# Kernel optimization log

Measured on AMD Instinct MI355X. Metric: run time of the kernel, lower is better.

## Reference

```python
import jax, jax.numpy as jnp
import numpy as np

N_NODES = 100000
N_EDGES = 1200000
N_GRAPHS = 256
IN_DIM = 15
HID = 64


def setup_inputs() -> dict:
    key = jax.random.key(0)
    ks = jax.random.split(key, 12)
    x = jax.random.normal(ks[0], (N_NODES, IN_DIM), dtype=jnp.float32)
    edge_index = jax.random.randint(ks[1], (2, N_EDGES), 0, N_NODES, dtype=jnp.int64)
    batch = jnp.sort(jax.random.randint(ks[2], (N_NODES,), 0, N_GRAPHS, dtype=jnp.int64))
    def glorot(k, fan_in, fan_out):
        lim = jnp.sqrt(6.0 / (fan_in + fan_out)).astype(jnp.float32)
        return jax.random.uniform(k, (fan_in, fan_out), jnp.float32, -lim, lim)
    return {
        'x': x, 'edge_index': edge_index, 'batch': batch,
        'W1': glorot(ks[3], IN_DIM, HID), 'b1': jnp.zeros((HID,), jnp.float32),
        'W2': glorot(ks[4], HID, HID),    'b2': jnp.zeros((HID,), jnp.float32),
        'W3': glorot(ks[5], HID, HID),    'b3': jnp.zeros((HID,), jnp.float32),
        'W4': glorot(ks[6], HID, HID),    'b4': jnp.zeros((HID,), jnp.float32),
    }


def _gcn_conv(x, src, dst, norm, W, b):
    # GCNConv: h = x @ W; out[dst] += norm * h[src]; out += b
    h = x @ W                      # [N, out]
    msg = h[src] * norm[:, None]   # [E+N, out] gather + scale
    out = jax.ops.segment_sum(msg, dst, num_segments=N_NODES)
    return out + b


def reference(x, edge_index, batch, W1, b1, W2, b2, W3, b3, W4, b4):
    # gcn_norm with self-loops (PyG default): A_hat = D^-1/2 (A+I) D^-1/2
    loop = jnp.arange(N_NODES, dtype=edge_index.dtype)
    src = jnp.concatenate([edge_index[0], loop])
    dst = jnp.concatenate([edge_index[1], loop])
    deg = jax.ops.segment_sum(jnp.ones_like(src, dtype=x.dtype), dst, num_segments=N_NODES)
    dinv = jnp.where(deg > 0, jax.lax.rsqrt(deg), 0.0)
    norm = dinv[src] * dinv[dst]   # [E+N]

    h = jax.nn.relu(_gcn_conv(x, src, dst, norm, W1, b1))
    h = jax.nn.relu(_gcn_conv(h, src, dst, norm, W2, b2))
    h = jax.nn.relu(_gcn_conv(h, src, dst, norm, W3, b3))
    h = jax.nn.relu(_gcn_conv(h, src, dst, norm, W4, b4))

    # global_mean_pool over batch ids
    sums = jax.ops.segment_sum(h, batch, num_segments=N_GRAPHS)
    cnt = jax.ops.segment_sum(jnp.ones((N_NODES,), h.dtype), batch, num_segments=N_GRAPHS)
    return sums / jnp.maximum(cnt, 1.0)[:, None]
```

## Files before the change

### kernel.cpp

```cpp
#include <hip/hip_runtime.h>
#include <hip/hip_bf16.h>

#define NN 100000
#define NE 1200000
#define NG 256
#define NB 256
#define BSZ 391
#define NBK1 128
#define ECH 9376
#define MAXB 6144
#define NBND_BLK 391
#define NPAD_BLK 6250

typedef __attribute__((ext_vector_type(8))) short bf16x8;
typedef __attribute__((ext_vector_type(4))) float f32x4;

__device__ __forceinline__ unsigned f2b(float f) {
    unsigned b = __float_as_uint(f);
    return (b + 0x7FFFu + ((b >> 16) & 1u)) >> 16;
}
__device__ __forceinline__ float b2f(unsigned short u) {
    return __uint_as_float((unsigned)u << 16);
}
__device__ __forceinline__ float4 b2f4(ushort4 u) {
    return make_float4(b2f(u.x), b2f(u.y), b2f(u.z), b2f(u.w));
}
__device__ __forceinline__ void add_u4(float* a, uint4 v) {
    const unsigned* u = (const unsigned*)&v;
#pragma unroll
    for (int i = 0; i < 4; ++i) {
        a[2*i]   += __uint_as_float(u[i] << 16);
        a[2*i+1] += __uint_as_float(u[i] & 0xFFFF0000u);
    }
}

__global__ void ph0_hist(const int* __restrict__ dst, int* __restrict__ hrows) {
    __shared__ int h[NB];
    const int t = threadIdx.x;
    h[t] = 0;
    __syncthreads();
    const int e0 = blockIdx.x * ECH;
    const int cnt = min(ECH, NE - e0);
    for (int i = t; i < cnt; i += 256)
        atomicAdd(&h[dst[e0 + i] / BSZ], 1);
    __syncthreads();
    hrows[blockIdx.x * NB + t] = h[t];
}

__global__ void ph_scan(const int* __restrict__ hrows, int* __restrict__ chunkoff,
                        int* __restrict__ bbase, int* __restrict__ row_off) {
    __shared__ int s[NB];
    const int t = threadIdx.x;
    int run = 0;
    for (int b = 0; b < NBK1; ++b) {
        int v = hrows[b * NB + t];
        chunkoff[b * NB + t] = run;
        run += v;
    }
    s[t] = run;
    __syncthreads();
    for (int off = 1; off < NB; off <<= 1) {
        int u = (t >= off) ? s[t - off] : 0;
        __syncthreads();
        s[t] += u;
        __syncthreads();
    }
    const int excl = s[t] - run;
    bbase[t] = excl;
    for (int b = 0; b < NBK1; ++b) chunkoff[b * NB + t] += excl;
    if (t == NB - 1) { bbase[NB] = NE; row_off[NN] = NE; }
}

__global__ void ph1_bucketize(const int* __restrict__ src, const int* __restrict__ dst,
                              const int* __restrict__ chunkoff, unsigned* __restrict__ barray) {
    __shared__ int lbase[NB];
    __shared__ int lcur[NB];
    const int t = threadIdx.x;
    lbase[t] = chunkoff[blockIdx.x * NB + t];
    lcur[t] = 0;
    __syncthreads();
    const int e0 = blockIdx.x * ECH;
    const int cnt = min(ECH, NE - e0);
    for (int i = t; i < cnt; i += 256) {
        int d = dst[e0 + i], s = src[e0 + i];
        int b = d / BSZ;
        int pos = lbase[b] + atomicAdd(&lcur[b], 1);
        barray[pos] = ((unsigned)(d - b * BSZ) << 17) | (unsigned)s;
    }
}

__global__ void ph2_build(const unsigned* __restrict__ barray, const int* __restrict__ bbase,
                          int* __restrict__ row_off, float* __restrict__ dinv,
                          int* __restrict__ csr) {
    __shared__ unsigned estage[MAXB];
    __shared__ int lcsr[MAXB];
    __shared__ int s[512];
    __shared__ int cur[BSZ];
    const int t = threadIdx.x;
    const int b = blockIdx.x;
    const int ebase = bbase[b];
    const int cnt = bbase[b + 1] - ebase;
    const int nbase = b * BSZ;
    const int nnodes = min(BSZ, NN - nbase);
    s[t] = 0; s[t + 256] = 0;
    __syncthreads();
    for (int i = t; i < cnt; i += 256) {
        unsigned e = barray[ebase + i];
        estage[i] = e;
        atomicAdd(&s[e >> 17], 1);
    }
    __syncthreads();
    for (int off = 1; off < 512; off <<= 1) {
        int v1 = (t >= off) ? s[t - off] : 0;
        int v2 = s[t + 256 - off];
        __syncthreads();
        s[t] += v1; s[t + 256] += v2;
        __syncthreads();
    }
    for (int l = t; l < nnodes; l += 256) {
        int incl = s[l];
        int excl = l ? s[l - 1] : 0;
        row_off[nbase + l] = ebase + excl;
        dinv[nbase + l] = rsqrtf((float)(incl - excl) + 1.0f);
        cur[l] = excl;
    }
    __syncthreads();
    for (int i = t; i < cnt; i += 256) {
        unsigned e = estage[i];
        int pos = atomicAdd(&cur[e >> 17], 1);
        lcsr[pos] = (int)(e & 0x1FFFFu);
    }
    __syncthreads();
    for (int i = t; i < cnt; i += 256)
        csr[ebase + i] = lcsr[i];
}

__global__ void k_prep(const float* __restrict__ W2, const float* __restrict__ W3,
                       const float* __restrict__ W4, unsigned short* __restrict__ wt,
                       const float* __restrict__ x, const float* __restrict__ dinv,
                       unsigned short* __restrict__ xs,
                       const int* __restrict__ batch, int* __restrict__ gstart) {
    const int blk = blockIdx.x;
    const int t = threadIdx.x;
    if (blk < 3) {
        const float* W = (blk == 0) ? W2 : (blk == 1) ? W3 : W4;
        unsigned short* o = wt + blk * 8192;
        const int n = t >> 2;
        const int j0 = (t & 3) * 16;
#pragma unroll
        for (int j = 0; j < 16; ++j) {
            float wv = W[(j0 + j) * 64 + n];
            unsigned short h = (unsigned short)f2b(wv);
            o[n * 64 + j0 + j] = h;
            o[4096 + n * 64 + j0 + j] = (unsigned short)f2b(wv - b2f(h));
        }
    } else if (blk < 3 + NBND_BLK) {
        int i = (blk - 3) * 256 + t;
        if (i >= NN) return;
        int b = batch[i];
        if (i == 0) {
            for (int g = 0; g <= b; ++g) gstart[g] = 0;
        } else {
            int bp = batch[i - 1];
            for (int g = bp + 1; g <= b; ++g) gstart[g] = i;
        }
        if (i == NN - 1) {
            for (int g = b + 1; g <= NG; ++g) gstart[g] = NN;
        }
    } else {
        int i = (blk - 3 - NBND_BLK) * 256 + t;
        if (i < NN * 16) {
            int n = i >> 4, k = i & 15;
            float v = (k < 15) ? dinv[n] * x[n * 15 + k] : 0.f;
            xs[i] = (unsigned short)f2b(v);
        }
    }
}

__global__ void fused1(const unsigned short* __restrict__ xs, const int* __restrict__ row_off,
                       const int* __restrict__ csr, const float* __restrict__ dinv,
                       const float* __restrict__ W, const float* __restrict__ bias,
                       unsigned* __restrict__ out) {
    __shared__ float4 Wl[16][16];
    __shared__ float  al[64][20];
    const int t = threadIdx.x;
    if (t < 240) Wl[t >> 4][t & 15] = ((const float4*)W)[t];
    if (t < 16) Wl[15][t] = make_float4(0,0,0,0);
    const int nl = t >> 2, c4 = t & 3;
    const int node = blockIdx.x * 64 + nl;
    float4 acc = make_float4(0,0,0,0);
    float dv = 0.f;
    if (node < NN) {
        const ushort4* base = (const ushort4*)xs;
        acc = b2f4(base[(size_t)node * 4 + c4]);
        int p = row_off[node], e = row_off[node + 1];
        for (; p + 3 < e; p += 4) {
            int s0 = csr[p], s1 = csr[p+1], s2 = csr[p+2], s3 = csr[p+3];
            float4 a = b2f4(base[(size_t)s0 * 4 + c4]);
            float4 b = b2f4(base[(size_t)s1 * 4 + c4]);
            float4 c = b2f4(base[(size_t)s2 * 4 + c4]);
            float4 d = b2f4(base[(size_t)s3 * 4 + c4]);
            acc.x += (a.x + b.x) + (c.x + d.x);
            acc.y += (a.y + b.y) + (c.y + d.y);
            acc.z += (a.z + b.z) + (c.z + d.z);
            acc.w += (a.w + b.w) + (c.w + d.w);
        }
        for (; p < e; ++p) {
            float4 a = b2f4(base[(size_t)csr[p] * 4 + c4]);
            acc.x += a.x; acc.y += a.y; acc.z += a.z; acc.w += a.w;
        }
        dv = dinv[node];
        acc.x *= dv; acc.y *= dv; acc.z *= dv; acc.w *= dv;
    }
    ((float4*)&al[nl][0])[c4] = acc;
    __syncthreads();
    if (node >= NN) return;
    float4 o0 = ((const float4*)bias)[c4 * 4 + 0];
    float4 o1 = ((const float4*)bias)[c4 * 4 + 1];
    float4 o2 = ((const float4*)bias)[c4 * 4 + 2];
    float4 o3 = ((const float4*)bias)[c4 * 4 + 3];
#pragma unroll
    for (int k = 0; k < 16; ++k) {
        float a = al[nl][k];
        float4 w0 = Wl[k][c4 * 4 + 0];
        float4 w1 = Wl[k][c4 * 4 + 1];
        float4 w2 = Wl[k][c4 * 4 + 2];
        float4 w3 = Wl[k][c4 * 4 + 3];
        o0.x = fmaf(a, w0.x, o0.x); o0.y = fmaf(a, w0.y, o0.y); o0.z = fmaf(a, w0.z, o0.z); o0.w = fmaf(a, w0.w, o0.w);
        o1.x = fmaf(a, w1.x, o1.x); o1.y = fmaf(a, w1.y, o1.y); o1.z = fmaf(a, w1.z, o1.z); o1.w = fmaf(a, w1.w, o1.w);
        o2.x = fmaf(a, w2.x, o2.x); o2.y = fmaf(a, w2.y, o2.y); o2.z = fmaf(a, w2.z, o2.z); o2.w = fmaf(a, w2.w, o2.w);
        o3.x = fmaf(a, w3.x, o3.x); o3.y = fmaf(a, w3.y, o3.y); o3.z = fmaf(a, w3.z, o3.z); o3.w = fmaf(a, w3.w, o3.w);
    }
    float dv2 = dv;
    o0.x = fmaxf(o0.x, 0.f) * dv2; o0.y = fmaxf(o0.y, 0.f) * dv2; o0.z = fmaxf(o0.z, 0.f) * dv2; o0.w = fmaxf(o0.w, 0.f) * dv2;
    o1.x = fmaxf(o1.x, 0.f) * dv2; o1.y = fmaxf(o1.y, 0.f) * dv2; o1.z = fmaxf(o1.z, 0.f) * dv2; o1.w = fmaxf(o1.w, 0.f) * dv2;
    o2.x = fmaxf(o2.x, 0.f) * dv2; o2.y = fmaxf(o2.y, 0.f) * dv2; o2.z = fmaxf(o2.z, 0.f) * dv2; o2.w = fmaxf(o2.w, 0.f) * dv2;
    o3.x = fmaxf(o3.x, 0.f) * dv2; o3.y = fmaxf(o3.y, 0.f) * dv2; o3.z = fmaxf(o3.z, 0.f) * dv2; o3.w = fmaxf(o3.w, 0.f) * dv2;
    uint4 lo, hi;
    lo.x = f2b(o0.x) | (f2b(o0.y) << 16);
    lo.y = f2b(o0.z) | (f2b(o0.w) << 16);
    lo.z = f2b(o1.x) | (f2b(o1.y) << 16);
    lo.w = f2b(o1.z) | (f2b(o1.w) << 16);
    hi.x = f2b(o2.x) | (f2b(o2.y) << 16);
    hi.y = f2b(o2.z) | (f2b(o2.w) << 16);
    hi.z = f2b(o3.x) | (f2b(o3.y) << 16);
    hi.w = f2b(o3.z) | (f2b(o3.w) << 16);
    uint4* ob = (uint4*)out + (size_t)node * 8 + c4 * 2;
    ob[0] = lo; ob[1] = hi;
}

template <bool LAST>
__global__ __launch_bounds__(256) void fused64(const unsigned short* __restrict__ g,
                        const int* __restrict__ row_off, const int* __restrict__ csr,
                        const float* __restrict__ dinv, const unsigned short* __restrict__ wt,
                        const float* __restrict__ bias, void* __restrict__ outv) {
    __shared__ alignas(16) unsigned short Ahi[16][72];
    __shared__ alignas(16) unsigned short Alo[16][72];
    __shared__ alignas(16) float dinv_l[16];
    const int t = threadIdx.x;

    const int nl = t >> 4;
    const int s8 = (t >> 3) & 1;
    const int q  = t & 7;
    const int node = blockIdx.x * 16 + nl;
    float acc[8] = {0,0,0,0,0,0,0,0};
    const float dv = dinv[node];
    {
        const uint4* fbase = (const uint4*)g;
        const int r0 = row_off[node], r1 = row_off[node + 1];
        const int half = (r1 - r0 + 1) >> 1;
        int p = r0 + s8 * half;
        const int e = s8 ? r1 : (r0 + half);
        if (s8 == 0) add_u4(acc, fbase[(size_t)node * 8 + q]);
        int i0 = csr[p],   i1 = csr[p+1], i2 = csr[p+2], i3 = csr[p+3];
        int i4 = csr[p+4], i5 = csr[p+5], i6 = csr[p+6], i7 = csr[p+7];
        while (p < e) {
            const int rem = e - p;
            uint4 v0, v1, v2, v3, v4, v5, v6, v7;
            v0 = fbase[(size_t)i0 * 8 + q];
            if (rem > 1) v1 = fbase[(size_t)i1 * 8 + q];
            if (rem > 2) v2 = fbase[(size_t)i2 * 8 + q];
            if (rem > 3) v3 = fbase[(size_t)i3 * 8 + q];
            if (rem > 4) v4 = fbase[(size_t)i4 * 8 + q];
            if (rem > 5) v5 = fbase[(size_t)i5 * 8 + q];
            if (rem > 6) v6 = fbase[(size_t)i6 * 8 + q];
            if (rem > 7) v7 = fbase[(size_t)i7 * 8 + q];
            p += 8;
            i0 = csr[p];   i1 = csr[p+1]; i2 = csr[p+2]; i3 = csr[p+3];
            i4 = csr[p+4]; i5 = csr[p+5]; i6 = csr[p+6]; i7 = csr[p+7];
            add_u4(acc, v0);
            if (rem > 1) add_u4(acc, v1);
            if (rem > 2) add_u4(acc, v2);
            if (rem > 3) add_u4(acc, v3);
            if (rem > 4) add_u4(acc, v4);
            if (rem > 5) add_u4(acc, v5);
            if (rem > 6) add_u4(acc, v6);
            if (rem > 7) add_u4(acc, v7);
        }
    }
#pragma unroll
    for (int i = 0; i < 8; ++i) acc[i] += __shfl_xor(acc[i], 8, 64);
    if (s8 == 0) {
        uint4 uh, ul;
        unsigned* uhp = (unsigned*)&uh;
        unsigned* ulp = (unsigned*)&ul;
#pragma unroll
        for (int i = 0; i < 4; ++i) {
            float va = acc[2*i] * dv;
            float vb = acc[2*i+1] * dv;
            unsigned ha = f2b(va), hb = f2b(vb);
            unsigned la = f2b(va - b2f((unsigned short)ha));
            unsigned lb = f2b(vb - b2f((unsigned short)hb));
            uhp[i] = ha | (hb << 16);
            ulp[i] = la | (lb << 16);
        }
        *(uint4*)&Ahi[nl][q * 8] = uh;
        *(uint4*)&Alo[nl][q * 8] = ul;
        if (q == 0) dinv_l[nl] = dv;
    }
    const int wid = t >> 6;
    const int l = t & 63;
    const int rr = l & 15;
    const int kb = l >> 4;
    const unsigned short* wrow = wt + (wid * 16 + rr) * 64;
    bf16x8 bh0 = *(const bf16x8*)(wrow + kb * 8);
    bf16x8 bh1 = *(const bf16x8*)(wrow + 32 + kb * 8);
    bf16x8 bl0 = *(const bf16x8*)(wrow + 4096 + kb * 8);
    bf16x8 bl1 = *(const bf16x8*)(wrow + 4096 + 32 + kb * 8);
    __syncthreads();

    f32x4 c = {0.f, 0.f, 0.f, 0.f};
    {
        bf16x8 ah0 = *(const bf16x8*)&Ahi[rr][kb * 8];
        bf16x8 am0 = *(const bf16x8*)&Alo[rr][kb * 8];
        c = __builtin_amdgcn_mfma_f32_16x16x32_bf16(ah0, bh0, c, 0, 0, 0);
        c = __builtin_amdgcn_mfma_f32_16x16x32_bf16(ah0, bl0, c, 0, 0, 0);
        c = __builtin_amdgcn_mfma_f32_16x16x32_bf16(am0, bh0, c, 0, 0, 0);
        bf16x8 ah1 = *(const bf16x8*)&Ahi[rr][32 + kb * 8];
        bf16x8 am1 = *(const bf16x8*)&Alo[rr][32 + kb * 8];
        c = __builtin_amdgcn_mfma_f32_16x16x32_bf16(ah1, bh1, c, 0, 0, 0);
        c = __builtin_amdgcn_mfma_f32_16x16x32_bf16(ah1, bl1, c, 0, 0, 0);
        c = __builtin_amdgcn_mfma_f32_16x16x32_bf16(am1, bh1, c, 0, 0, 0);
    }
    float bv = bias[wid * 16 + rr];
    float4 dq = *(const float4*)&dinv_l[kb * 4];
    const float* dqp = (const float*)&dq;
#pragma unroll
    for (int r = 0; r < 4; ++r) {
        int nd = blockIdx.x * 16 + kb * 4 + r;
        float o = fmaxf(c[r] + bv, 0.f);
        if (!LAST) {
            o *= dqp[r];
            ((unsigned short*)outv)[(size_t)nd * 64 + wid * 16 + rr] = (unsigned short)f2b(o);
        } else {
            ((float*)outv)[(size_t)nd * 64 + wid * 16 + rr] = o;
        }
    }
}

__global__ void k_pool(const float* __restrict__ h, const int* __restrict__ gstart,
                       float* __restrict__ out) {
    __shared__ float s[4][64];
    int g = blockIdx.x;
    int t = threadIdx.x, lane = t & 63, w = t >> 6;
    int r0 = gstart[g], r1 = gstart[g + 1];
    float acc = 0.f;
    for (int r = r0 + w; r < r1; r += 4) acc += h[(size_t)r * 64 + lane];
    s[w][lane] = acc;
    __syncthreads();
    if (t < 64) {
        float v = s[0][t] + s[1][t] + s[2][t] + s[3][t];
        float c = (float)(r1 - r0);
        out[g * 64 + t] = v / fmaxf(c, 1.f);
    }
}

static inline size_t al256(size_t x) { return (x + 255) & ~(size_t)255; }

extern "C" void kernel_launch(void* const* d_in, const int* in_sizes, int n_in,
                              void* d_out, int out_size, void* d_ws, size_t ws_size,
                              hipStream_t stream) {
    const float* x     = (const float*)d_in[0];
    const int*   eidx  = (const int*)d_in[1];
    const int*   batch = (const int*)d_in[2];
    const float* W1 = (const float*)d_in[3];  const float* b1 = (const float*)d_in[4];
    const float* W2 = (const float*)d_in[5];  const float* b2 = (const float*)d_in[6];
    const float* W3 = (const float*)d_in[7];  const float* b3 = (const float*)d_in[8];
    const float* W4 = (const float*)d_in[9];  const float* b4 = (const float*)d_in[10];
    float* out = (float*)d_out;
    (void)in_sizes; (void)n_in; (void)out_size; (void)ws_size;

    const int* src = eidx;
    const int* dst = eidx + NE;

    char* p = (char*)d_ws;
    size_t off = 0;
    int*   hrows   = (int*)(p + off);   off = al256(off + sizeof(int) * NBK1 * NB);
    int*   chunkoff= (int*)(p + off);   off = al256(off + sizeof(int) * NBK1 * NB);
    int*   bbase   = (int*)(p + off);   off = al256(off + sizeof(int) * (NB + 1));
    int*   gstart  = (int*)(p + off);   off = al256(off + sizeof(int) * (NG + 1));
    int*   row_off = (int*)(p + off);   off = al256(off + sizeof(int) * (NN + 1));
    float* dinv    = (float*)(p + off); off = al256(off + sizeof(float) * NN);
    unsigned short* wt = (unsigned short*)(p + off); off = al256(off + sizeof(short) * 3 * 8192);
    int*   csr     = (int*)(p + off);   off = al256(off + sizeof(int) * (NE + 16));
    unsigned short* F0 = (unsigned short*)(p + off); off = al256(off + sizeof(short) * (size_t)NN * 64);
    unsigned short* F1 = (unsigned short*)(p + off); off = al256(off + sizeof(short) * (size_t)NN * 64);
    float* H4      = (float*)(p + off); off = al256(off + sizeof(float) * (size_t)NN * 64);
    unsigned*       barray = (unsigned*)H4;
    unsigned short* xs     = F1;

    ph0_hist     <<<NBK1, 256, 0, stream>>>(dst, hrows);
    ph_scan      <<<1, NB, 0, stream>>>(hrows, chunkoff, bbase, row_off);
    ph1_bucketize<<<NBK1, 256, 0, stream>>>(src, dst, chunkoff, barray);
    ph2_build    <<<NB, 256, 0, stream>>>(barray, bbase, row_off, dinv, csr);
    k_prep       <<<3 + NBND_BLK + NPAD_BLK, 256, 0, stream>>>(W2, W3, W4, wt, x, dinv, xs, batch, gstart);

    fused1        <<<(NN + 63) / 64, 256, 0, stream>>>(xs, row_off, csr, dinv, W1, b1, (unsigned*)F0);
    fused64<false><<<NN / 16, 256, 0, stream>>>(F0, row_off, csr, dinv, wt,        b2, F1);
    fused64<false><<<NN / 16, 256, 0, stream>>>(F1, row_off, csr, dinv, wt + 8192, b3, F0);
    fused64<true> <<<NN / 16, 256, 0, stream>>>(F0, row_off, csr, dinv, wt + 16384,b4, H4);

    k_pool  <<<NG, 256, 0, stream>>>(H4, gstart, out);
}
```

Before: 208.2 us.

## Parallelize bucket offset scan and stage weights in LDS for fused64

The single-block serial scan over 128 chunk histograms is split into a 256-block parallel column scan plus a small second-level scan. Bucketize now adds the bucket base to each chunk offset itself. Separately, fused64 cooperatively copies the full hi/lo bf16 weight matrix into padded shared memory and has each wave read its MFMA B operands from LDS rather than from per-lane global loads. This adds one kernel launch and about 18KB of LDS per block, which may reduce occupancy of the gather-heavy fused kernels.

```diff
diff --git a/kernel.cpp b/kernel.cpp
--- a/kernel.cpp
+++ b/kernel.cpp
@@ -47,17 +47,30 @@
     hrows[blockIdx.x * NB + t] = h[t];
 }
 
-__global__ void ph_scan(const int* __restrict__ hrows, int* __restrict__ chunkoff,
-                        int* __restrict__ bbase, int* __restrict__ row_off) {
+__global__ void ph_scanA(const int* __restrict__ hrows, int* __restrict__ chunkoff,
+                         int* __restrict__ btot) {
+    __shared__ int s[NBK1];
+    const int b = threadIdx.x;
+    const int t = blockIdx.x;
+    int v = hrows[b * NB + t];
+    s[b] = v;
+    __syncthreads();
+    for (int off = 1; off < NBK1; off <<= 1) {
+        int u = (b >= off) ? s[b - off] : 0;
+        __syncthreads();
+        s[b] += u;
+        __syncthreads();
+    }
+    chunkoff[b * NB + t] = s[b] - v;
+    if (b == NBK1 - 1) btot[t] = s[b];
+}
+
+__global__ void ph_scanB(const int* __restrict__ btot, int* __restrict__ bbase,
+                         int* __restrict__ row_off) {
     __shared__ int s[NB];
     const int t = threadIdx.x;
-    int run = 0;
-    for (int b = 0; b < NBK1; ++b) {
-        int v = hrows[b * NB + t];
-        chunkoff[b * NB + t] = run;
-        run += v;
-    }
-    s[t] = run;
+    int v = btot[t];
+    s[t] = v;
     __syncthreads();
     for (int off = 1; off < NB; off <<= 1) {
         int u = (t >= off) ? s[t - off] : 0;
@@ -65,18 +78,17 @@
         s[t] += u;
         __syncthreads();
     }
-    const int excl = s[t] - run;
-    bbase[t] = excl;
-    for (int b = 0; b < NBK1; ++b) chunkoff[b * NB + t] += excl;
+    bbase[t] = s[t] - v;
     if (t == NB - 1) { bbase[NB] = NE; row_off[NN] = NE; }
 }
 
 __global__ void ph1_bucketize(const int* __restrict__ src, const int* __restrict__ dst,
-                              const int* __restrict__ chunkoff, unsigned* __restrict__ barray) {
+                              const int* __restrict__ chunkoff, const int* __restrict__ bbase,
+                              unsigned* __restrict__ barray) {
     __shared__ int lbase[NB];
     __shared__ int lcur[NB];
     const int t = threadIdx.x;
-    lbase[t] = chunkoff[blockIdx.x * NB + t];
+    lbase[t] = bbase[t] + chunkoff[blockIdx.x * NB + t];
     lcur[t] = 0;
     __syncthreads();
     const int e0 = blockIdx.x * ECH;
@@ -256,8 +268,23 @@
                         const float* __restrict__ bias, void* __restrict__ outv) {
     __shared__ alignas(16) unsigned short Ahi[16][72];
     __shared__ alignas(16) unsigned short Alo[16][72];
+    __shared__ alignas(16) unsigned short Bhi[64][72];
+    __shared__ alignas(16) unsigned short Blo[64][72];
     __shared__ alignas(16) float dinv_l[16];
     const int t = threadIdx.x;
+
+    {
+        const uint4* srcv = (const uint4*)wt;
+#pragma unroll
+        for (int i = 0; i < 4; ++i) {
+            int idx = t + i * 256;
+            uint4 v = srcv[idx];
+            int sel = idx >> 9, r = idx & 511;
+            int n = r >> 3, kc = r & 7;
+            unsigned short* dstp = sel ? &Blo[n][kc * 8] : &Bhi[n][kc * 8];
+            *(uint4*)dstp = v;
+        }
+    }
 
     const int nl = t >> 4;
     const int s8 = (t >> 3) & 1;
@@ -318,29 +345,22 @@
         *(uint4*)&Alo[nl][q * 8] = ul;
         if (q == 0) dinv_l[nl] = dv;
     }
+    __syncthreads();
+
     const int wid = t >> 6;
     const int l = t & 63;
     const int rr = l & 15;
     const int kb = l >> 4;
-    const unsigned short* wrow = wt + (wid * 16 + rr) * 64;
-    bf16x8 bh0 = *(const bf16x8*)(wrow + kb * 8);
-    bf16x8 bh1 = *(const bf16x8*)(wrow + 32 + kb * 8);
-    bf16x8 bl0 = *(const bf16x8*)(wrow + 4096 + kb * 8);
-    bf16x8 bl1 = *(const bf16x8*)(wrow + 4096 + 32 + kb * 8);
-    __syncthreads();
-
     f32x4 c = {0.f, 0.f, 0.f, 0.f};
-    {
-        bf16x8 ah0 = *(const bf16x8*)&Ahi[rr][kb * 8];
-        bf16x8 am0 = *(const bf16x8*)&Alo[rr][kb * 8];
-        c = __builtin_amdgcn_mfma_f32_16x16x32_bf16(ah0, bh0, c, 0, 0, 0);
-        c = __builtin_amdgcn_mfma_f32_16x16x32_bf16(ah0, bl0, c, 0, 0, 0);
-        c = __builtin_amdgcn_mfma_f32_16x16x32_bf16(am0, bh0, c, 0, 0, 0);
-        bf16x8 ah1 = *(const bf16x8*)&Ahi[rr][32 + kb * 8];
-        bf16x8 am1 = *(const bf16x8*)&Alo[rr][32 + kb * 8];
-        c = __builtin_amdgcn_mfma_f32_16x16x32_bf16(ah1, bh1, c, 0, 0, 0);
-        c = __builtin_amdgcn_mfma_f32_16x16x32_bf16(ah1, bl1, c, 0, 0, 0);
-        c = __builtin_amdgcn_mfma_f32_16x16x32_bf16(am1, bh1, c, 0, 0, 0);
+#pragma unroll
+    for (int ks = 0; ks < 2; ++ks) {
+        bf16x8 ah = *(const bf16x8*)&Ahi[rr][ks * 32 + kb * 8];
+        bf16x8 am = *(const bf16x8*)&Alo[rr][ks * 32 + kb * 8];
+        bf16x8 bh = *(const bf16x8*)&Bhi[wid * 16 + rr][ks * 32 + kb * 8];
+        bf16x8 bl = *(const bf16x8*)&Blo[wid * 16 + rr][ks * 32 + kb * 8];
+        c = __builtin_amdgcn_mfma_f32_16x16x32_bf16(ah, bh, c, 0, 0, 0);
+        c = __builtin_amdgcn_mfma_f32_16x16x32_bf16(ah, bl, c, 0, 0, 0);
+        c = __builtin_amdgcn_mfma_f32_16x16x32_bf16(am, bh, c, 0, 0, 0);
     }
     float bv = bias[wid * 16 + rr];
     float4 dq = *(const float4*)&dinv_l[kb * 4];
@@ -397,6 +417,7 @@
     size_t off = 0;
     int*   hrows   = (int*)(p + off);   off = al256(off + sizeof(int) * NBK1 * NB);
     int*   chunkoff= (int*)(p + off);   off = al256(off + sizeof(int) * NBK1 * NB);
+    int*   btot    = (int*)(p + off);   off = al256(off + sizeof(int) * NB);
     int*   bbase   = (int*)(p + off);   off = al256(off + sizeof(int) * (NB + 1));
     int*   gstart  = (int*)(p + off);   off = al256(off + sizeof(int) * (NG + 1));
     int*   row_off = (int*)(p + off);   off = al256(off + sizeof(int) * (NN + 1));
@@ -410,8 +431,9 @@
     unsigned short* xs     = F1;
 
     ph0_hist     <<<NBK1, 256, 0, stream>>>(dst, hrows);
-    ph_scan      <<<1, NB, 0, stream>>>(hrows, chunkoff, bbase, row_off);
-    ph1_bucketize<<<NBK1, 256, 0, stream>>>(src, dst, chunkoff, barray);
+    ph_scanA     <<<NB, NBK1, 0, stream>>>(hrows, chunkoff, btot);
+    ph_scanB     <<<1, NB, 0, stream>>>(btot, bbase, row_off);
+    ph1_bucketize<<<NBK1, 256, 0, stream>>>(src, dst, chunkoff, bbase, barray);
     ph2_build    <<<NB, 256, 0, stream>>>(barray, bbase, row_off, dinv, csr);
     k_prep       <<<3 + NBND_BLK + NPAD_BLK, 256, 0, stream>>>(W2, W3, W4, wt, x, dinv, xs, batch, gstart);
 
```

Result: faster. 180.7 us, median of 2 (-13.2%).
